# Optimization experiments

Hardware: AMD Instinct MI355X
Metric: run time of the kernel (lower is better)

Reference implementation:

```python
import jax, jax.numpy as jnp
import numpy as np

# region/recall params from layer config
NUM_CLASSES = 20
NUM_ANCHORS = 5
ANCHORS = jnp.array([[1.3221, 1.73145], [3.19275, 4.00944], [5.05587, 8.09892],
                     [9.47112, 4.84053], [11.2364, 10.0071]], dtype=jnp.float32)
CONF_THRESH = 0.5
NMS_THRESH = 0.45
IOU_THRESH = 0.5
EPS = 1e-6


def setup_inputs() -> dict:
    key = jax.random.key(0)
    k1, k2 = jax.random.split(key)
    output = jax.random.normal(k1, (8, NUM_ANCHORS * (5 + NUM_CLASSES), 19, 19), dtype=jnp.float32)
    target = jax.random.uniform(k2, (8, 250), dtype=jnp.float32)  # [B, 50*5] rows: cls,cx,cy,w,h
    return {"output": output, "target": target}


def decode_region_boxes(output):
    """get_region_boxes: anchor decode. output [B, A*(5+C), H, W] -> boxes [B, A*H*W, 4] cxcywh (normalized), det_conf [B, A*H*W]."""
    B, _, H, W = output.shape
    o = output.reshape(B, NUM_ANCHORS, 5 + NUM_CLASSES, H, W)
    gx = jnp.arange(W, dtype=output.dtype)
    gy = jnp.arange(H, dtype=output.dtype)
    cx = (jax.nn.sigmoid(o[:, :, 0]) + gx[None, None, None, :]) / W
    cy = (jax.nn.sigmoid(o[:, :, 1]) + gy[None, None, :, None]) / H
    bw = jnp.exp(o[:, :, 2]) * (ANCHORS[:, 0] / W)[None, :, None, None]
    bh = jnp.exp(o[:, :, 3]) * (ANCHORS[:, 1] / H)[None, :, None, None]
    det_conf = jax.nn.sigmoid(o[:, :, 4])
    boxes = jnp.stack([cx, cy, bw, bh], axis=-1).reshape(B, -1, 4)
    return boxes, det_conf.reshape(B, -1)


def pairwise_iou(a, b):
    """bbox_iou(x1y1x2y2=False) for all pairs. a [..., Na, 4], b [..., Nb, 4] cxcywh -> [..., Na, Nb]."""
    ax1 = (a[..., 0] - a[..., 2] * 0.5)[..., :, None]
    ax2 = (a[..., 0] + a[..., 2] * 0.5)[..., :, None]
    ay1 = (a[..., 1] - a[..., 3] * 0.5)[..., :, None]
    ay2 = (a[..., 1] + a[..., 3] * 0.5)[..., :, None]
    bx1 = (b[..., 0] - b[..., 2] * 0.5)[..., None, :]
    bx2 = (b[..., 0] + b[..., 2] * 0.5)[..., None, :]
    by1 = (b[..., 1] - b[..., 3] * 0.5)[..., None, :]
    by2 = (b[..., 1] + b[..., 3] * 0.5)[..., None, :]
    uw = jnp.maximum(ax2, bx2) - jnp.minimum(ax1, bx1)
    uh = jnp.maximum(ay2, by2) - jnp.minimum(ay1, by1)
    aw = a[..., 2][..., :, None]; ah = a[..., 3][..., :, None]
    bw = b[..., 2][..., None, :]; bh = b[..., 3][..., None, :]
    cw = aw + bw - uw
    ch = ah + bh - uh
    carea = jnp.where((cw > 0) & (ch > 0), cw * ch, 0.0)
    uarea = aw * ah + bw * bh - carea
    return carea / uarea


def greedy_nms_keep(iou_mat, valid):
    """Sequential greedy NMS over conf-sorted boxes using precomputed IoU. iou_mat [N,N], valid [N] bool."""
    N = valid.shape[0]
    idx = jnp.arange(N)
    def body(i, keep):
        sup = keep[i] & (iou_mat[i] > NMS_THRESH) & (idx > i)
        return keep & (~sup)
    return jax.lax.fori_loop(0, N, body, valid)


def reference(output, target):
    B = output.shape[0]
    boxes, det = decode_region_boxes(output)              # [B,N,4], [B,N]
    # sort by det_conf descending (nms sort order)
    order = jnp.argsort(-det, axis=1)
    boxes = jnp.take_along_axis(boxes, order[..., None], axis=1)
    det = jnp.take_along_axis(det, order, axis=1)
    valid = det > CONF_THRESH                             # boxes that enter nms (conf filter in get_region_boxes)
    iou_mat = pairwise_iou(boxes, boxes)                  # [B,N,N]
    keep = jax.vmap(greedy_nms_keep)(iou_mat, valid)      # [B,N]
    proposals = jnp.sum(keep)
    # ground truth: [B,T,5] rows [cls,cx,cy,w,h]; num_gts = boxes until first cx==0
    truths = target.reshape(B, -1, 5)
    gt_valid = jnp.cumprod((truths[..., 1] != 0).astype(jnp.int32), axis=1).astype(bool)  # [B,T]
    total = jnp.sum(gt_valid)
    iou_gt = pairwise_iou(truths[..., 1:5], boxes)        # [B,T,N]
    best_iou = jnp.max(jnp.where(keep[:, None, :], iou_gt, 0.0), axis=-1)  # [B,T]
    correct = jnp.sum(gt_valid & (best_iou > IOU_THRESH))
    total_f = total.astype(jnp.float32)
    prop_f = proposals.astype(jnp.float32)
    corr_f = correct.astype(jnp.float32)
    precision = corr_f / (prop_f + EPS)
    recall = corr_f / (total_f + EPS)
    fscore = 2.0 * precision * recall / (precision + recall + EPS)
    return jnp.stack([total_f, prop_f, corr_f, precision, recall, fscore])
```

## Files before the change

### kernel.cpp

```cpp
#include <hip/hip_runtime.h>

namespace {
constexpr int NA    = 5;
constexpr int NCELL = 361;
constexpr int NBOX  = 1805;
constexpr int NBOXP = 1856;
constexpr int NT1   = 256;
constexpr int TMAX  = 50;
constexpr float CONF_T = 0.5f;
constexpr float NMS_T  = 0.45f;
constexpr float IOU_T  = 0.5f;
constexpr int NWMAX   = 32;
constexpr int ROWPAD  = 1856;
constexpr int SOA_STRIDE = NBOXP;
constexpr int SOA_ARR    = 8 * SOA_STRIDE;
constexpr size_t WS_PART = 0;
constexpr size_t WS_M    = 128;
constexpr size_t WS_SOA  = 256;
constexpr size_t WS_SUP  = 360448;
}

__device__ __constant__ float d_anchw[NA] = {1.3221f, 3.19275f, 5.05587f, 9.47112f, 11.2364f};
__device__ __constant__ float d_anchh[NA] = {1.73145f, 4.00944f, 8.09892f, 4.84053f, 10.0071f};

__device__ inline unsigned long long shflx64(unsigned long long v, int m) {
    int lo = __shfl_xor((int)(unsigned)(v & 0xffffffffull), m, 64);
    int hi = __shfl_xor((int)(unsigned)(v >> 32), m, 64);
    return ((unsigned long long)(unsigned)hi << 32) | (unsigned)lo;
}
__device__ inline unsigned long long rdlane64(unsigned long long v, int l) {
    unsigned lo = (unsigned)__builtin_amdgcn_readlane((int)(unsigned)(v & 0xffffffffull), l);
    unsigned hi = (unsigned)__builtin_amdgcn_readlane((int)(unsigned)(v >> 32), l);
    return ((unsigned long long)hi << 32) | lo;
}
__device__ inline void barrier_lgkm() {
    __asm__ volatile("" ::: "memory");
    __builtin_amdgcn_s_waitcnt(0xC07F);
    __builtin_amdgcn_s_barrier();
    __asm__ volatile("" ::: "memory");
}

__global__ __launch_bounds__(NT1, 1) void k_decode_sort(
    const float* __restrict__ net, float* __restrict__ soa,
    int* __restrict__ Marr)
{
    __shared__ unsigned long long skey[2048];
    __shared__ float4 sbox[NBOX];
    __shared__ int sCnt;
    const int b = blockIdx.x, tid = threadIdx.x, lane = tid & 63;
    const float* op = net + (size_t)b * (NA * 25 * NCELL);
    if (tid == 0) sCnt = 0;
    __syncthreads();

    for (int n = tid; n < NBOX; n += NT1) {
        int a = n / NCELL;
        int r = n - a * NCELL;
        int y = r / 19;
        int x = r - y * 19;
        int base = a * 25 * NCELL + r;
        float t0 = op[base];
        float t1 = op[base + 1 * NCELL];
        float t2 = op[base + 2 * NCELL];
        float t3 = op[base + 3 * NCELL];
        float t4 = op[base + 4 * NCELL];
        float cx = (1.0f / (1.0f + expf(-t0)) + (float)x) / 19.0f;
        float cy = (1.0f / (1.0f + expf(-t1)) + (float)y) / 19.0f;
        float bw = expf(t2) * (d_anchw[a] / 19.0f);
        float bh = expf(t3) * (d_anchh[a] / 19.0f);
        float det = 1.0f / (1.0f + expf(-t4));
        sbox[n] = make_float4(cx, cy, bw, bh);
        bool valid = det > CONF_T;
        unsigned long long bm = __ballot(valid);
        int base0 = 0;
        if (lane == 0 && bm) base0 = atomicAdd(&sCnt, __popcll(bm));
        base0 = __shfl(base0, 0, 64);
        if (valid) {
            int pos = base0 + __popcll(bm & ((1ull << lane) - 1ull));
            skey[pos] = ((unsigned long long)(~__float_as_uint(det)) << 32) | (unsigned)n;
        }
    }
    __syncthreads();
    const int M = sCnt;
    int S = 64; while (S < M) S <<= 1;
    for (int n = M + tid; n < S; n += NT1) skey[n] = ~0ull;
    __syncthreads();

    unsigned long long v[8];
    const int nt8 = S >> 3;
    const int base8 = tid << 3;
    auto cas = [&](int xx, int yy, bool up) {
        unsigned long long a = v[xx], c = v[yy];
        if ((a > c) == up) { v[xx] = c; v[yy] = a; }
    };
    if (tid < nt8) {
        #pragma unroll
        for (int p = 0; p < 8; ++p) v[p] = skey[base8 + p];
        cas(0,1,true); cas(2,3,false); cas(4,5,true); cas(6,7,false);
        cas(0,2,true); cas(1,3,true); cas(4,6,false); cas(5,7,false);
        cas(0,1,true); cas(2,3,true); cas(4,5,false); cas(6,7,false);
        bool u8 = ((base8 & 8) == 0);
        cas(0,4,u8); cas(1,5,u8); cas(2,6,u8); cas(3,7,u8);
        cas(0,2,u8); cas(1,3,u8); cas(4,6,u8); cas(5,7,u8);
        cas(0,1,u8); cas(2,3,u8); cas(4,5,u8); cas(6,7,u8);
        #pragma unroll
        for (int p = 0; p < 8; ++p) skey[base8 + p] = v[p];
    }
    __syncthreads();
    for (unsigned k = 16; k <= (unsigned)S; k <<= 1) {
        for (unsigned j = k >> 1; j >= 8; j >>= 1) {
            for (unsigned m = tid; m < (unsigned)(S >> 1); m += NT1) {
                unsigned i = ((m & ~(j - 1)) << 1) | (m & (j - 1));
                unsigned p = i | j;
                bool up = ((i & k) == 0);
                unsigned long long a = skey[i], c2 = skey[p];
                if ((a > c2) == up) { skey[i] = c2; skey[p] = a; }
            }
            __syncthreads();
        }
        if (tid < nt8) {
            #pragma unroll
            for (int p = 0; p < 8; ++p) v[p] = skey[base8 + p];
            bool up = ((base8 & k) == 0);
            cas(0,4,up); cas(1,5,up); cas(2,6,up); cas(3,7,up);
            cas(0,2,up); cas(1,3,up); cas(4,6,up); cas(5,7,up);
            cas(0,1,up); cas(2,3,up); cas(4,5,up); cas(6,7,up);
            #pragma unroll
            for (int p = 0; p < 8; ++p) skey[base8 + p] = v[p];
        }
        __syncthreads();
    }

    float* X1 = soa + 0 * SOA_ARR + b * SOA_STRIDE;
    float* Y1 = soa + 1 * SOA_ARR + b * SOA_STRIDE;
    float* X2 = soa + 2 * SOA_ARR + b * SOA_STRIDE;
    float* Y2 = soa + 3 * SOA_ARR + b * SOA_STRIDE;
    float* Wd = soa + 4 * SOA_ARR + b * SOA_STRIDE;
    float* Hd = soa + 5 * SOA_ARR + b * SOA_STRIDE;
    const int mceil = (M + 63) & ~63;
    for (int p = tid; p < mceil; p += NT1) {
        float4 bx = make_float4(0.f, 0.f, 0.f, 0.f);
        if (p < M) bx = sbox[(unsigned)(skey[p] & 0xffffffffull)];
        X1[p] = bx.x - 0.5f * bx.z;
        Y1[p] = bx.y - 0.5f * bx.w;
        X2[p] = bx.x + 0.5f * bx.z;
        Y2[p] = bx.y + 0.5f * bx.w;
        Wd[p] = bx.z;
        Hd[p] = bx.w;
    }
    if (tid == 0) Marr[b] = M;
}

__global__ __launch_bounds__(256) void k_iou_maskT(
    const float* __restrict__ soa, const int* __restrict__ Marr,
    unsigned long long* __restrict__ supT)
{
    const int blk  = blockIdx.x;
    const int b    = blk & 7;
    const int g    = blk >> 3;
    const int wv   = threadIdx.x >> 6;
    const int lane = threadIdx.x & 63;
    const int M = Marr[b];
    const int i0 = g * 16 + wv * 4;
    if (i0 >= M) return;
    const float* X1 = soa + 0 * SOA_ARR + b * SOA_STRIDE;
    const float* Y1 = soa + 1 * SOA_ARR + b * SOA_STRIDE;
    const float* X2 = soa + 2 * SOA_ARR + b * SOA_STRIDE;
    const float* Y2 = soa + 3 * SOA_ARR + b * SOA_STRIDE;
    const float* Wd = soa + 4 * SOA_ARR + b * SOA_STRIDE;
    const float* Hd = soa + 5 * SOA_ARR + b * SOA_STRIDE;
    const int nch = (M + 63) >> 6;
    const int w0  = i0 >> 6;

    float ax1[4], ay1[4], ax2[4], ay2[4], aw[4], ah[4], aarea[4];
    #pragma unroll
    for (int r = 0; r < 4; ++r) {
        int ir = i0 + r; if (ir >= M) ir = M - 1;
        ax1[r] = X1[ir]; ay1[r] = Y1[ir];
        ax2[r] = X2[ir]; ay2[r] = Y2[ir];
        aw[r]  = Wd[ir]; ah[r]  = Hd[ir];
        aarea[r] = aw[r] * ah[r];
    }
    unsigned long long myw0 = 0, myw1 = 0, myw2 = 0, myw3 = 0;
    for (int w = w0; w < nch; ++w) {
        int j = (w << 6) + lane;
        float bx1 = X1[j], by1 = Y1[j];
        float bx2 = X2[j], by2 = Y2[j];
        float bw  = Wd[j], bh  = Hd[j];
        float barea = bw * bh;
        bool jok = (j < M);
        #pragma unroll
        for (int r = 0; r < 4; ++r) {
            bool pred = false;
            if (jok && j > i0 + r) {
                float uw = fmaxf(ax2[r], bx2) - fminf(ax1[r], bx1);
                float uh = fmaxf(ay2[r], by2) - fminf(ay1[r], by1);
                float cw = aw[r] + bw - uw;
                float ch = ah[r] + bh - uh;
                if (cw > 0.0f && ch > 0.0f) {
                    float ca = cw * ch;
                    float ua = aarea[r] + barea - ca;
                    pred = ca > NMS_T * ua;
                }
            }
            unsigned long long m = __ballot(pred);
            if (w == lane) {
                if      (r == 0) myw0 = m;
                else if (r == 1) myw1 = m;
                else if (r == 2) myw2 = m;
                else             myw3 = m;
            }
        }
    }
    if (lane >= w0 && lane < nch) {
        unsigned long long* dst = supT + ((size_t)b * 32 + lane) * ROWPAD;
        dst[i0] = myw0;
        if (i0 + 1 < M) dst[i0 + 1] = myw1;
        if (i0 + 2 < M) dst[i0 + 2] = myw2;
        if (i0 + 3 < M) dst[i0 + 3] = myw3;
    }
}

__global__ __launch_bounds__(1024, 1) void k_sweep(
    const float* __restrict__ soa, const float* __restrict__ tgt,
    const int* __restrict__ Marr, const unsigned long long* __restrict__ supT,
    int* __restrict__ partials)
{
    __shared__ float X1s[NBOXP], Y1s[NBOXP], X2s[NBOXP], Y2s[NBOXP];
    __shared__ float Wss[NBOXP], Hss[NBOXP];
    __shared__ unsigned long long rmw[NWMAX], keepw[NWMAX];
    __shared__ int sNV, sCorr, sProp;
    const int b = blockIdx.x, tid = threadIdx.x;
    const int wv = tid >> 6, lane = tid & 63;
    const int M = Marr[b];
    const int nwa = (M + 63) >> 6;
    const unsigned long long* sb = supT + (size_t)b * 32 * ROWPAD;

    if (tid < NWMAX) { rmw[tid] = 0ull; keepw[tid] = 0ull; }
    if (tid == 0) { sCorr = 0; sProp = 0; }

    {
        int mceil = (M + 63) & ~63;
        const float* X1 = soa + 0 * SOA_ARR + b * SOA_STRIDE;
        const float* Y1 = soa + 1 * SOA_ARR + b * SOA_STRIDE;
        const float* X2 = soa + 2 * SOA_ARR + b * SOA_STRIDE;
        const float* Y2 = soa + 3 * SOA_ARR + b * SOA_STRIDE;
        const float* Wd = soa + 4 * SOA_ARR + b * SOA_STRIDE;
        const float* Hd = soa + 5 * SOA_ARR + b * SOA_STRIDE;
        for (int p = tid; p < mceil; p += 1024) {
            X1s[p] = X1[p]; Y1s[p] = Y1[p];
            X2s[p] = X2[p]; Y2s[p] = Y2[p];
            Wss[p] = Wd[p]; Hss[p] = Hd[p];
        }
    }
    if (wv == 2) {
        float cxv = (lane < TMAX) ? tgt[b * 250 + lane * 5 + 1] : 0.0f;
        unsigned long long bm = __ballot(cxv != 0.0f);
        unsigned long long inv = (~bm) & ((1ull << TMAX) - 1ull);
        if (lane == 0) sNV = inv ? (__ffsll((long long)inv) - 1) : TMAX;
    }

    const int w1 = (wv >= 1) ? wv : -1;
    const int w2 = (wv >= 1 && wv + 15 <= 28) ? (wv + 15) : -1;
    unsigned long long cur1 = 0, cur2 = 0, diag = 0;
    if (wv == 0 && nwa > 0) diag = sb[lane];
    if (w1 >= 1 && w1 < nwa) cur1 = sb[(size_t)w1 * ROWPAD + lane];
    if (w2 >= 1 && w2 < nwa) cur2 = sb[(size_t)w2 * ROWPAD + lane];
    __syncthreads();

    for (int t = 0; t < nwa; ++t) {
        if (wv == 0) {
            unsigned long long cur = rmw[t];
            int rem = M - (t << 6);
            unsigned long long vm = (rem >= 64) ? ~0ull : ((1ull << rem) - 1ull);
            unsigned long long live = vm & ~cur;
            while (live) {
                int i = __ffsll((long long)live) - 1;
                unsigned long long w64 = rdlane64(diag, i);
                cur |= w64;
                live &= ~w64;
                live &= ~(1ull << i);
            }
            unsigned long long kp = vm & ~cur;
            if (lane == 0) keepw[t] = kp;
            int tn = t + 1;
            if (tn < nwa) diag = sb[(size_t)tn * ROWPAD + (tn << 6) + lane];
        }
        barrier_lgkm();
        {
            unsigned long long kmt = keepw[t];
            if (w1 > t && w1 < nwa) {
                unsigned long long c = ((kmt >> lane) & 1ull) ? cur1 : 0ull;
                c |= shflx64(c, 1);  c |= shflx64(c, 2);  c |= shflx64(c, 4);
                c |= shflx64(c, 8);  c |= shflx64(c, 16); c |= shflx64(c, 32);
                if (lane == 0) rmw[w1] |= c;
            }
            if (w2 > t && w2 < nwa) {
                unsigned long long c = ((kmt >> lane) & 1ull) ? cur2 : 0ull;
                c |= shflx64(c, 1);  c |= shflx64(c, 2);  c |= shflx64(c, 4);
                c |= shflx64(c, 8);  c |= shflx64(c, 16); c |= shflx64(c, 32);
                if (lane == 0) rmw[w2] |= c;
            }
            if (w1 > t + 1 && w1 < nwa) cur1 = sb[(size_t)w1 * ROWPAD + ((t + 1) << 6) + lane];
            if (w2 > t + 1 && w2 < nwa) cur2 = sb[(size_t)w2 * ROWPAD + ((t + 1) << 6) + lane];
        }
        barrier_lgkm();
    }

    if (wv == 0) {
        unsigned long long kv = (lane < NWMAX) ? keepw[lane] : 0ull;
        int pc = __popcll(kv);
        for (int d = 32; d > 0; d >>= 1) pc += __shfl_down(pc, d, 64);
        if (lane == 0) sProp = pc;
    }

    const int nv = sNV;
    for (int t = wv; t < nv; t += 16) {
        const float* g = tgt + b * 250 + t * 5;
        float gcx = g[1], gcy = g[2], gw = g[3], gh = g[4];
        float gx1 = gcx - 0.5f * gw, gx2 = gcx + 0.5f * gw;
        float gy1 = gcy - 0.5f * gh, gy2 = gcy + 0.5f * gh;
        float garea = gw * gh;
        float best = 0.0f;
        for (int j0 = 0; j0 < M; j0 += 64) {
            unsigned long long kw = keepw[j0 >> 6];
            if (kw == 0ull) continue;
            int j = j0 + lane;
            bool ok = (j < M) && ((kw >> lane) & 1ull);
            int js = (j < NBOXP) ? j : (NBOXP - 1);
            float bw = Wss[js], bh = Hss[js];
            float uw = fmaxf(gx2, X2s[js]) - fminf(gx1, X1s[js]);
            float uh = fmaxf(gy2, Y2s[js]) - fminf(gy1, Y1s[js]);
            float cww = gw + bw - uw, chh = gh + bh - uh;
            float ca = (cww > 0.0f && chh > 0.0f) ? cww * chh : 0.0f;
            float ua = garea + bw * bh - ca;
            float iou = ca / ua;
            best = fmaxf(best, ok ? iou : 0.0f);
        }
        for (int d = 32; d > 0; d >>= 1) best = fmaxf(best, __shfl_down(best, d, 64));
        if (lane == 0 && best > IOU_T) atomicAdd(&sCorr, 1);
    }
    barrier_lgkm();

    if (tid == 0) {
        partials[b * 4 + 0] = sProp;
        partials[b * 4 + 1] = sCorr;
        partials[b * 4 + 2] = sNV;
    }
}

__global__ __launch_bounds__(64) void k_final(
    const int* __restrict__ partials, float* __restrict__ out)
{
    const int lane = threadIdx.x;
    int p = 0, c = 0, t = 0;
    if (lane < 8) {
        p = partials[lane * 4 + 0];
        c = partials[lane * 4 + 1];
        t = partials[lane * 4 + 2];
    }
    for (int d = 4; d > 0; d >>= 1) {
        p += __shfl_down(p, d, 64);
        c += __shfl_down(c, d, 64);
        t += __shfl_down(t, d, 64);
    }
    if (lane == 0) {
        float prop  = (float)p;
        float corr  = (float)c;
        float total = (float)t;
        float prec = corr / (prop + 1e-6f);
        float rec  = corr / (total + 1e-6f);
        float fs   = 2.0f * prec * rec / (prec + rec + 1e-6f);
        out[0] = total;
        out[1] = prop;
        out[2] = corr;
        out[3] = prec;
        out[4] = rec;
        out[5] = fs;
    }
}

extern "C" void kernel_launch(void* const* d_in, const int* in_sizes, int n_in,
                              void* d_out, int out_size, void* d_ws, size_t ws_size,
                              hipStream_t stream) {
    const float* net = (const float*)d_in[0];
    const float* tgt = (const float*)d_in[1];
    char* ws = (char*)d_ws;
    int* partials = (int*)(ws + WS_PART);
    int* Marr     = (int*)(ws + WS_M);
    float* soa    = (float*)(ws + WS_SOA);
    unsigned long long* supT = (unsigned long long*)(ws + WS_SUP);

    k_decode_sort<<<8, NT1, 0, stream>>>(net, soa, Marr);
    int rowblocks = (NBOX + 15) / 16;
    k_iou_maskT<<<rowblocks * 8, 256, 0, stream>>>(soa, Marr, supT);
    k_sweep<<<8, 1024, 0, stream>>>(soa, tgt, Marr, supT, partials);
    k_final<<<1, 64, 0, stream>>>(partials, (float*)d_out);
}
```

Measured before the change: 134.8 us.

## Halve NMS sweep barriers via lookahead carry and fuse final reduction into sweep

The sweep loop now has one barrier per step instead of two. Wave 0 also reads the suppression words of the next column block and passes them forward as a carry. The other waves only update blocks at least two steps ahead, so no race remains on the row mask. The separate final kernel is removed: each block atomically adds its counts into zeroed counters, and the last block to finish computes and writes the metrics. This saves one launch and a dependency, at the cost of extra readlanes in the serial loop and global atomics.

```diff
diff --git a/kernel.cpp b/kernel.cpp
--- a/kernel.cpp
+++ b/kernel.cpp
@@ -14,10 +14,10 @@
 constexpr int ROWPAD  = 1856;
 constexpr int SOA_STRIDE = NBOXP;
 constexpr int SOA_ARR    = 8 * SOA_STRIDE;
-constexpr size_t WS_PART = 0;
-constexpr size_t WS_M    = 128;
-constexpr size_t WS_SOA  = 256;
-constexpr size_t WS_SUP  = 360448;
+constexpr size_t WS_COUNT = 0;
+constexpr size_t WS_M     = 64;
+constexpr size_t WS_SOA   = 256;
+constexpr size_t WS_SUP   = 360448;
 }
 
 __device__ __constant__ float d_anchw[NA] = {1.3221f, 3.19275f, 5.05587f, 9.47112f, 11.2364f};
@@ -42,7 +42,7 @@
 
 __global__ __launch_bounds__(NT1, 1) void k_decode_sort(
     const float* __restrict__ net, float* __restrict__ soa,
-    int* __restrict__ Marr)
+    int* __restrict__ Marr, int* __restrict__ counters)
 {
     __shared__ unsigned long long skey[2048];
     __shared__ float4 sbox[NBOX];
@@ -50,6 +50,7 @@
     const int b = blockIdx.x, tid = threadIdx.x, lane = tid & 63;
     const float* op = net + (size_t)b * (NA * 25 * NCELL);
     if (tid == 0) sCnt = 0;
+    if (b == 0 && tid < 4) counters[tid] = 0;
     __syncthreads();
 
     for (int n = tid; n < NBOX; n += NT1) {
@@ -223,7 +224,7 @@
 __global__ __launch_bounds__(1024, 1) void k_sweep(
     const float* __restrict__ soa, const float* __restrict__ tgt,
     const int* __restrict__ Marr, const unsigned long long* __restrict__ supT,
-    int* __restrict__ partials)
+    int* __restrict__ counters, float* __restrict__ out)
 {
     __shared__ float X1s[NBOXP], Y1s[NBOXP], X2s[NBOXP], Y2s[NBOXP];
     __shared__ float Wss[NBOXP], Hss[NBOXP];
@@ -261,49 +262,58 @@
 
     const int w1 = (wv >= 1) ? wv : -1;
     const int w2 = (wv >= 1 && wv + 15 <= 28) ? (wv + 15) : -1;
-    unsigned long long cur1 = 0, cur2 = 0, diag = 0;
-    if (wv == 0 && nwa > 0) diag = sb[lane];
-    if (w1 >= 1 && w1 < nwa) cur1 = sb[(size_t)w1 * ROWPAD + lane];
-    if (w2 >= 1 && w2 < nwa) cur2 = sb[(size_t)w2 * ROWPAD + lane];
+    unsigned long long cur1 = 0, cur2 = 0, diag = 0, colnext = 0, carry = 0;
+    if (wv == 0 && nwa > 0) {
+        diag = sb[lane];
+        if (nwa > 1) colnext = sb[(size_t)1 * ROWPAD + lane];
+    }
+    if (w1 >= 2 && w1 < nwa) cur1 = sb[(size_t)w1 * ROWPAD + lane];
+    if (w2 >= 2 && w2 < nwa) cur2 = sb[(size_t)w2 * ROWPAD + lane];
     __syncthreads();
 
     for (int t = 0; t < nwa; ++t) {
         if (wv == 0) {
-            unsigned long long cur = rmw[t];
+            unsigned long long cur = rmw[t] | carry;
             int rem = M - (t << 6);
             unsigned long long vm = (rem >= 64) ? ~0ull : ((1ull << rem) - 1ull);
             unsigned long long live = vm & ~cur;
+            unsigned long long nxt = 0;
             while (live) {
                 int i = __ffsll((long long)live) - 1;
                 unsigned long long w64 = rdlane64(diag, i);
+                unsigned long long nx  = rdlane64(colnext, i);
                 cur |= w64;
+                nxt |= nx;
                 live &= ~w64;
                 live &= ~(1ull << i);
             }
-            unsigned long long kp = vm & ~cur;
-            if (lane == 0) keepw[t] = kp;
+            if (lane == 0) keepw[t] = vm & ~cur;
+            carry = nxt;
             int tn = t + 1;
-            if (tn < nwa) diag = sb[(size_t)tn * ROWPAD + (tn << 6) + lane];
+            if (tn < nwa) {
+                diag = sb[(size_t)tn * ROWPAD + (tn << 6) + lane];
+                colnext = (tn + 1 < nwa)
+                    ? sb[(size_t)(tn + 1) * ROWPAD + (tn << 6) + lane] : 0ull;
+            }
         }
         barrier_lgkm();
         {
             unsigned long long kmt = keepw[t];
-            if (w1 > t && w1 < nwa) {
+            if (w1 > t + 1 && w1 < nwa) {
                 unsigned long long c = ((kmt >> lane) & 1ull) ? cur1 : 0ull;
                 c |= shflx64(c, 1);  c |= shflx64(c, 2);  c |= shflx64(c, 4);
                 c |= shflx64(c, 8);  c |= shflx64(c, 16); c |= shflx64(c, 32);
                 if (lane == 0) rmw[w1] |= c;
             }
-            if (w2 > t && w2 < nwa) {
+            if (w2 > t + 1 && w2 < nwa) {
                 unsigned long long c = ((kmt >> lane) & 1ull) ? cur2 : 0ull;
                 c |= shflx64(c, 1);  c |= shflx64(c, 2);  c |= shflx64(c, 4);
                 c |= shflx64(c, 8);  c |= shflx64(c, 16); c |= shflx64(c, 32);
                 if (lane == 0) rmw[w2] |= c;
             }
-            if (w1 > t + 1 && w1 < nwa) cur1 = sb[(size_t)w1 * ROWPAD + ((t + 1) << 6) + lane];
-            if (w2 > t + 1 && w2 < nwa) cur2 = sb[(size_t)w2 * ROWPAD + ((t + 1) << 6) + lane];
-        }
-        barrier_lgkm();
+            if (w1 > t + 2 && w1 < nwa) cur1 = sb[(size_t)w1 * ROWPAD + ((t + 1) << 6) + lane];
+            if (w2 > t + 2 && w2 < nwa) cur2 = sb[(size_t)w2 * ROWPAD + ((t + 1) << 6) + lane];
+        }
     }
 
     if (wv == 0) {
@@ -342,40 +352,25 @@
     barrier_lgkm();
 
     if (tid == 0) {
-        partials[b * 4 + 0] = sProp;
-        partials[b * 4 + 1] = sCorr;
-        partials[b * 4 + 2] = sNV;
-    }
-}
-
-__global__ __launch_bounds__(64) void k_final(
-    const int* __restrict__ partials, float* __restrict__ out)
-{
-    const int lane = threadIdx.x;
-    int p = 0, c = 0, t = 0;
-    if (lane < 8) {
-        p = partials[lane * 4 + 0];
-        c = partials[lane * 4 + 1];
-        t = partials[lane * 4 + 2];
-    }
-    for (int d = 4; d > 0; d >>= 1) {
-        p += __shfl_down(p, d, 64);
-        c += __shfl_down(c, d, 64);
-        t += __shfl_down(t, d, 64);
-    }
-    if (lane == 0) {
-        float prop  = (float)p;
-        float corr  = (float)c;
-        float total = (float)t;
-        float prec = corr / (prop + 1e-6f);
-        float rec  = corr / (total + 1e-6f);
-        float fs   = 2.0f * prec * rec / (prec + rec + 1e-6f);
-        out[0] = total;
-        out[1] = prop;
-        out[2] = corr;
-        out[3] = prec;
-        out[4] = rec;
-        out[5] = fs;
+        atomicAdd(counters + 0, sProp);
+        atomicAdd(counters + 1, sCorr);
+        atomicAdd(counters + 2, sNV);
+        __threadfence();
+        int done = atomicAdd(counters + 3, 1);
+        if (done == 7) {
+            float prop  = (float)atomicAdd(counters + 0, 0);
+            float corr  = (float)atomicAdd(counters + 1, 0);
+            float total = (float)atomicAdd(counters + 2, 0);
+            float prec = corr / (prop + 1e-6f);
+            float rec  = corr / (total + 1e-6f);
+            float fs   = 2.0f * prec * rec / (prec + rec + 1e-6f);
+            out[0] = total;
+            out[1] = prop;
+            out[2] = corr;
+            out[3] = prec;
+            out[4] = rec;
+            out[5] = fs;
+        }
     }
 }
 
@@ -385,14 +380,13 @@
     const float* net = (const float*)d_in[0];
     const float* tgt = (const float*)d_in[1];
     char* ws = (char*)d_ws;
-    int* partials = (int*)(ws + WS_PART);
+    int* counters = (int*)(ws + WS_COUNT);
     int* Marr     = (int*)(ws + WS_M);
     float* soa    = (float*)(ws + WS_SOA);
     unsigned long long* supT = (unsigned long long*)(ws + WS_SUP);
 
-    k_decode_sort<<<8, NT1, 0, stream>>>(net, soa, Marr);
+    k_decode_sort<<<8, NT1, 0, stream>>>(net, soa, Marr, counters);
     int rowblocks = (NBOX + 15) / 16;
     k_iou_maskT<<<rowblocks * 8, 256, 0, stream>>>(soa, Marr, supT);
-    k_sweep<<<8, 1024, 0, stream>>>(soa, tgt, Marr, supT, partials);
-    k_final<<<1, 64, 0, stream>>>(partials, (float*)d_out);
-}
+    k_sweep<<<8, 1024, 0, stream>>>(soa, tgt, Marr, supT, counters, (float*)d_out);
+}
```

New measurement: 149.1 us. 10.6% more time.
